# Performance work log

Hardware: AMD Instinct MI355X
Metric: run time of the kernel (lower is better)

Reference implementation:

```python
import jax, jax.numpy as jnp
import numpy as np

NSAMPLE = 3  # three_nn default
EPS = 1e-10
CLAMP = 10.0


def setup_inputs() -> dict:
    key = jax.random.key(0)
    k1, k2, k3 = jax.random.split(key, 3)
    B, C, N = 4, 3, 8192
    pos1 = jax.random.normal(k1, (B, C, N), dtype=jnp.float32)
    pos2 = jax.random.normal(k2, (B, C, N), dtype=jnp.float32)
    flow1 = jax.random.normal(k3, (B, C, N), dtype=jnp.float32) * 0.1
    return {"pos1": pos1, "pos2": pos2, "flow1": flow1}


def reference(pos1, pos2, flow1):
    # pos1, flow1: [B,3,N1]; pos2: [B,3,N2]
    pos1_to_2 = pos1 + flow1                       # warped source points [B,3,N1]
    q = jnp.transpose(pos2, (0, 2, 1))             # queries  [B,N2,3]
    k = jnp.transpose(pos1_to_2, (0, 2, 1))        # database [B,N1,3]

    # brute-force 3-NN: squared distances [B,N2,N1]
    d2 = (jnp.sum(q * q, axis=-1, keepdims=True)
          - 2.0 * jnp.einsum('bqc,bnc->bqn', q, k)
          + jnp.sum(k * k, axis=-1)[:, None, :])
    _, knn_idx = jax.lax.top_k(-d2, NSAMPLE)       # [B,N2,NSAMPLE] into N1

    # gather neighbor coords: [B,N2,NSAMPLE,3]
    grouped_pts = jax.vmap(lambda pts, ii: pts[ii])(k, knn_idx)
    diff = grouped_pts - q[:, :, None, :]
    dist = jnp.maximum(jnp.linalg.norm(diff, axis=-1), EPS)  # [B,N2,NSAMPLE]
    inv = 1.0 / dist
    weight = inv / jnp.sum(inv, axis=-1, keepdims=True)      # [B,N2,NSAMPLE]

    # gather neighbor flows and do inverse-distance-weighted average
    flow_t = jnp.transpose(flow1, (0, 2, 1))                 # [B,N1,3]
    grouped_flow = jax.vmap(lambda f, ii: f[ii])(flow_t, knn_idx)  # [B,N2,NSAMPLE,3]
    flow2 = jnp.sum(weight[..., None] * grouped_flow, axis=2)      # [B,N2,3]

    warped = pos2 - jnp.transpose(flow2, (0, 2, 1))          # [B,3,N2]
    return jnp.clip(warped, -CLAMP, CLAMP)
```

## Files before the change

### kernel.cpp

```cpp
#include <hip/hip_runtime.h>
#include <math.h>


#define BB 4
#define NN 8192
#define NC 30
#define NCELLS (NC * NC * NC)
#define NCT (BB * NCELLS)
#define GRID_R 3.3f
#define GRID_INVH (1.0f / 0.22f)
#define D3_THR (0.44f * 0.44f * 0.999f)
#define EPB 1024
#define SB 106

typedef unsigned long long u64;

__device__ __forceinline__ int cell_of(float x) {
  int c = (int)floorf((x + GRID_R) * GRID_INVH);
  return min(max(c, 0), NC - 1);
}

__device__ __forceinline__ void merge3(u64& a0, u64& a1, u64& a2,
                                       u64 b0, u64 b1, u64 b2) {
  const u64 lo0 = a0 < b0 ? a0 : b0;
  const u64 hi0 = a0 < b0 ? b0 : a0;
  const u64 lo1 = a1 < b1 ? a1 : b1;
  const u64 lo2 = a2 < b2 ? a2 : b2;
  const u64 o1 = hi0 < lo1 ? hi0 : lo1;
  const u64 t = hi0 < lo1 ? lo1 : hi0;
  a0 = lo0;
  a1 = o1;
  a2 = t < lo2 ? t : lo2;
}

__device__ __forceinline__ void insert3(u64& s0, u64& s1, u64& s2, u64 key) {
  const bool c0 = key < s0;
  const bool c1 = key < s1;
  const bool c2 = key < s2;
  s2 = c1 ? s1 : (c2 ? key : s2);
  s1 = c0 ? s0 : (c1 ? key : s1);
  s0 = c0 ? key : s0;
}

__global__ __launch_bounds__(256) void k_count(const float* __restrict__ p1,
                                               const float* __restrict__ f1,
                                               int* __restrict__ counts) {
  const int gid = blockIdx.x * 256 + threadIdx.x;
  const int b = gid >> 13, n = gid & (NN - 1);
  const float* P = p1 + (size_t)b * 3 * NN;
  const float* F = f1 + (size_t)b * 3 * NN;
  const float x = P[n] + F[n];
  const float y = P[NN + n] + F[NN + n];
  const float z = P[2 * NN + n] + F[2 * NN + n];
  const int cid = (cell_of(z) * NC + cell_of(y)) * NC + cell_of(x);
  atomicAdd(&counts[b * NCELLS + cid], 1);
}

__global__ __launch_bounds__(256) void k_scan1(int* __restrict__ counts,
                                               int* __restrict__ offs,
                                               int* __restrict__ partials) {
  __shared__ int wsums[4];
  const int tid = threadIdx.x, lane = tid & 63, wav = tid >> 6;
  const int c = blockIdx.x * EPB + tid * 4;
  int4 v = make_int4(0, 0, 0, 0);
  if (c < NCT) {
    v = *reinterpret_cast<const int4*>(counts + c);
    *reinterpret_cast<int4*>(counts + c) = make_int4(0, 0, 0, 0);
  }
  const int sum4 = v.x + v.y + v.z + v.w;
  int incl = sum4;
  for (int off = 1; off < 64; off <<= 1) {
    const int t = __shfl_up(incl, off, 64);
    incl += (lane >= off) ? t : 0;
  }
  if (lane == 63) wsums[wav] = incl;
  __syncthreads();
  int wbase = 0;
#pragma unroll
  for (int w = 0; w < 4; ++w) wbase += (w < wav) ? wsums[w] : 0;
  const int excl = wbase + incl - sum4;
  if (c < NCT) {
    int4 e;
    e.x = excl;
    e.y = excl + v.x;
    e.z = e.y + v.y;
    e.w = e.z + v.z;
    *reinterpret_cast<int4*>(offs + c) = e;
  }
  if (tid == 255) partials[blockIdx.x] = wbase + incl;
}

__global__ __launch_bounds__(128) void k_scan2(int* __restrict__ partials,
                                               int* __restrict__ offs) {
  __shared__ int w0sum;
  const int t = threadIdx.x, lane = t & 63, wav = t >> 6;
  const int v = (t < SB) ? partials[t] : 0;
  int incl = v;
  for (int off = 1; off < 64; off <<= 1) {
    const int u = __shfl_up(incl, off, 64);
    incl += (lane >= off) ? u : 0;
  }
  if (t == 63) w0sum = incl;
  __syncthreads();
  const int base = wav ? w0sum : 0;
  const int excl = base + incl - v;
  if (t < SB) partials[t] = excl;
  if (t == SB - 1) offs[NCT] = BB * NN - excl;
}

__global__ __launch_bounds__(256) void k_scatter(const float* __restrict__ p1,
                                                 const float* __restrict__ f1,
                                                 int* __restrict__ counts,
                                                 const int* __restrict__ offs,
                                                 const int* __restrict__ partials,
                                                 float4* __restrict__ csr) {
  const int gid = blockIdx.x * 256 + threadIdx.x;
  const int b = gid >> 13, n = gid & (NN - 1);
  const float* P = p1 + (size_t)b * 3 * NN;
  const float* F = f1 + (size_t)b * 3 * NN;
  const float x = P[n] + F[n];
  const float y = P[NN + n] + F[NN + n];
  const float z = P[2 * NN + n] + F[2 * NN + n];
  const int cid = (cell_of(z) * NC + cell_of(y)) * NC + cell_of(x);
  const int g = b * NCELLS + cid;
  const int rank = atomicAdd(&counts[g], 1);
  const int base = offs[g] + partials[g >> 10];
  csr[base + rank] = make_float4(x, y, z, __int_as_float(n));
}

__global__ __launch_bounds__(256) void k_query(const float* __restrict__ p1,
                                               const float* __restrict__ p2,
                                               const float* __restrict__ f1,
                                               const int* __restrict__ offs,
                                               const int* __restrict__ partials,
                                               const float4* __restrict__ csr,
                                               float* __restrict__ out) {
  __shared__ int cumL[4][32];
  __shared__ int adjL[4][32];
  const int tid = threadIdx.x, lane = tid & 63, wav = tid >> 6;
  const int bid = blockIdx.x;
  const int b = bid >> 11;
  const int qn = ((bid & 2047) << 2) | wav;
  const float* P1 = p1 + (size_t)b * 3 * NN;
  const float* P2 = p2 + (size_t)b * 3 * NN;
  const float* F1 = f1 + (size_t)b * 3 * NN;

  const float qx = P2[qn], qy = P2[NN + qn], qz = P2[2 * NN + qn];
  bool fb = !(fabsf(qx) < GRID_R && fabsf(qy) < GRID_R && fabsf(qz) < GRID_R);

  u64 s0 = ~0ULL, s1 = ~0ULL, s2 = ~0ULL;

  if (!fb) {
    const int qcx = cell_of(qx), qcy = cell_of(qy), qcz = cell_of(qz);
    int n_c = 0, start_c = 0;
    if (lane < 25) {
      const int gz = qcz + (lane / 5) - 2;
      const int gy = qcy + (lane % 5) - 2;
      if (gz >= 0 && gz < NC && gy >= 0 && gy < NC) {
        const int gxl = max(qcx - 2, 0), gxh = min(qcx + 2, NC - 1);
        const int cb = b * NCELLS + (gz * NC + gy) * NC;
        const int ia = cb + gxl, ib = cb + gxh + 1;
        start_c = offs[ia] + partials[ia >> 10];
        n_c = offs[ib] + partials[ib >> 10] - start_c;
      }
    }
    int incl = n_c;
    for (int off = 1; off < 64; off <<= 1) {
      const int v = __shfl_up(incl, off, 64);
      incl += (lane >= off) ? v : 0;
    }
    const int excl = incl - n_c;
    const int T = __shfl(incl, 24, 64);
    if (lane < 32) {
      cumL[wav][lane] = excl;
      adjL[wav][lane] = start_c - excl;
    }

    for (int g0 = 0; g0 < T; g0 += 64) {
      const int g = g0 + lane;
      const bool act = g < T;
      const int gg = act ? g : (T - 1);
      int c = 0;
#pragma unroll
      for (int st = 16; st >= 1; st >>= 1) {
        const int c2 = c + st;
        c = (cumL[wav][c2] <= gg) ? c2 : c;
      }
      const float4 pt = csr[adjL[wav][c] + gg];
      const float dx = pt.x - qx, dy = pt.y - qy, dz = pt.z - qz;
      const float d2 = fmaf(dx, dx, fmaf(dy, dy, dz * dz));
      u64 key = ((u64)__float_as_uint(d2) << 32) | (unsigned)__float_as_uint(pt.w);
      key = act ? key : ~0ULL;
      insert3(s0, s1, s2, key);
    }

#pragma unroll
    for (int mask = 32; mask >= 1; mask >>= 1) {
      const u64 b0 = __shfl_xor(s0, mask, 64);
      const u64 b1 = __shfl_xor(s1, mask, 64);
      const u64 b2 = __shfl_xor(s2, mask, 64);
      merge3(s0, s1, s2, b0, b1, b2);
    }

    const float d3 = __uint_as_float((unsigned)(s2 >> 32));
    fb = !(d3 <= D3_THR);
  }

  if (fb) {
    s0 = ~0ULL; s1 = ~0ULL; s2 = ~0ULL;
    for (int r = 0; r < NN / 64; ++r) {
      const int g = r * 64 + lane;
      const float x = P1[g] + F1[g];
      const float y = P1[NN + g] + F1[NN + g];
      const float z = P1[2 * NN + g] + F1[2 * NN + g];
      const float dx = x - qx, dy = y - qy, dz = z - qz;
      const float d2 = fmaf(dx, dx, fmaf(dy, dy, dz * dz));
      const u64 key = ((u64)__float_as_uint(d2) << 32) | (unsigned)g;
      insert3(s0, s1, s2, key);
    }
#pragma unroll
    for (int mask = 32; mask >= 1; mask >>= 1) {
      const u64 b0 = __shfl_xor(s0, mask, 64);
      const u64 b1 = __shfl_xor(s1, mask, 64);
      const u64 b2 = __shfl_xor(s2, mask, 64);
      merge3(s0, s1, s2, b0, b1, b2);
    }
  }

  if (lane == 0) {
    const int idxs[3] = {(int)(unsigned)s0 & (NN - 1),
                         (int)(unsigned)s1 & (NN - 1),
                         (int)(unsigned)s2 & (NN - 1)};
    float w[3], gfx[3], gfy[3], gfz[3];
    float wsumv = 0.0f;
#pragma unroll
    for (int r = 0; r < 3; ++r) {
      const int idx = idxs[r];
      const float fx = F1[idx], fy = F1[NN + idx], fz = F1[2 * NN + idx];
      const float kx = P1[idx] + fx;
      const float ky = P1[NN + idx] + fy;
      const float kz = P1[2 * NN + idx] + fz;
      const float dx = kx - qx, dy = ky - qy, dz = kz - qz;
      float d = sqrtf(dx * dx + dy * dy + dz * dz);
      d = fmaxf(d, 1e-10f);
      const float inv = 1.0f / d;
      w[r] = inv; wsumv += inv;
      gfx[r] = fx; gfy[r] = fy; gfz[r] = fz;
    }
    const float invw = 1.0f / wsumv;
    float ox = 0.0f, oy = 0.0f, oz = 0.0f;
#pragma unroll
    for (int r = 0; r < 3; ++r) {
      const float ww = w[r] * invw;
      ox = fmaf(ww, gfx[r], ox);
      oy = fmaf(ww, gfy[r], oy);
      oz = fmaf(ww, gfz[r], oz);
    }
    ox = qx - ox; oy = qy - oy; oz = qz - oz;
    ox = fminf(fmaxf(ox, -10.0f), 10.0f);
    oy = fminf(fmaxf(oy, -10.0f), 10.0f);
    oz = fminf(fmaxf(oz, -10.0f), 10.0f);
    float* o = out + (size_t)b * 3 * NN;
    o[qn] = ox;
    o[NN + qn] = oy;
    o[2 * NN + qn] = oz;
  }
}

extern "C" void kernel_launch(void* const* d_in, const int* in_sizes, int n_in,
                              void* d_out, int out_size, void* d_ws, size_t ws_size,
                              hipStream_t stream) {
  const float* pos1 = (const float*)d_in[0];
  const float* pos2 = (const float*)d_in[1];
  const float* flow1 = (const float*)d_in[2];
  float* out = (float*)d_out;

  char* ws = (char*)d_ws;
  int* counts = (int*)ws;
  int* offs = (int*)(ws + (size_t)NCT * 4);
  size_t part_off = ((size_t)NCT * 4 + ((size_t)NCT + 1) * 4 + 15) & ~(size_t)15;
  int* partials = (int*)(ws + part_off);
  size_t csr_off = (part_off + (size_t)SB * 4 + 15) & ~(size_t)15;
  float4* csr = (float4*)(ws + csr_off);

  hipMemsetAsync(counts, 0, (size_t)NCT * 4, stream);
  k_count<<<dim3(BB * NN / 256), dim3(256), 0, stream>>>(pos1, flow1, counts);
  k_scan1<<<dim3(SB), dim3(256), 0, stream>>>(counts, offs, partials);
  k_scan2<<<dim3(1), dim3(128), 0, stream>>>(partials, offs);
  k_scatter<<<dim3(BB * NN / 256), dim3(256), 0, stream>>>(pos1, flow1, counts, offs, partials, csr);
  k_query<<<dim3(BB * 2048), dim3(256), 0, stream>>>(pos1, pos2, flow1, offs, partials, csr, out);
}
```

Measured before the change: 86.21 us.

## Use four lanes per query and defer brute-force fallbacks to separate kernel

The query kernel now assigns four threads per query instead of a whole 64-lane wavefront, walking the 25 neighbouring cell rows with prefetch of the next row's offsets. Queries outside the grid or whose third-nearest distance fails the threshold are pushed onto a compacted queue via an atomic counter. A separate fallback kernel then brute-forces only those queries. Scan partials are folded into offsets by a new apply kernel, which removes the extra partials lookups. The intent is to cut the idle lanes and divergence of the wavefront-per-query design, at the cost of an extra launch and more serial work per thread.

```diff
diff --git a/kernel.cpp b/kernel.cpp
--- a/kernel.cpp
+++ b/kernel.cpp
@@ -40,6 +40,49 @@
   s2 = c1 ? s1 : (c2 ? key : s2);
   s1 = c0 ? s0 : (c1 ? key : s1);
   s0 = c0 ? key : s0;
+}
+
+__device__ __forceinline__ void idw_out(int b, int qn, float qx, float qy,
+                                        float qz, u64 s0, u64 s1, u64 s2,
+                                        const float* __restrict__ P1,
+                                        const float* __restrict__ F1,
+                                        float* __restrict__ out) {
+  const int idxs[3] = {(int)(unsigned)s0 & (NN - 1),
+                       (int)(unsigned)s1 & (NN - 1),
+                       (int)(unsigned)s2 & (NN - 1)};
+  float w[3], gfx[3], gfy[3], gfz[3];
+  float wsumv = 0.0f;
+#pragma unroll
+  for (int r = 0; r < 3; ++r) {
+    const int idx = idxs[r];
+    const float fx = F1[idx], fy = F1[NN + idx], fz = F1[2 * NN + idx];
+    const float kx = P1[idx] + fx;
+    const float ky = P1[NN + idx] + fy;
+    const float kz = P1[2 * NN + idx] + fz;
+    const float dx = kx - qx, dy = ky - qy, dz = kz - qz;
+    float d = sqrtf(dx * dx + dy * dy + dz * dz);
+    d = fmaxf(d, 1e-10f);
+    const float inv = 1.0f / d;
+    w[r] = inv; wsumv += inv;
+    gfx[r] = fx; gfy[r] = fy; gfz[r] = fz;
+  }
+  const float invw = 1.0f / wsumv;
+  float ox = 0.0f, oy = 0.0f, oz = 0.0f;
+#pragma unroll
+  for (int r = 0; r < 3; ++r) {
+    const float ww = w[r] * invw;
+    ox = fmaf(ww, gfx[r], ox);
+    oy = fmaf(ww, gfy[r], oy);
+    oz = fmaf(ww, gfz[r], oz);
+  }
+  ox = qx - ox; oy = qy - oy; oz = qz - oz;
+  ox = fminf(fmaxf(ox, -10.0f), 10.0f);
+  oy = fminf(fmaxf(oy, -10.0f), 10.0f);
+  oz = fminf(fmaxf(oz, -10.0f), 10.0f);
+  float* o = out + (size_t)b * 3 * NN;
+  o[qn] = ox;
+  o[NN + qn] = oy;
+  o[2 * NN + qn] = oz;
 }
 
 __global__ __launch_bounds__(256) void k_count(const float* __restrict__ p1,
@@ -90,8 +133,7 @@
   if (tid == 255) partials[blockIdx.x] = wbase + incl;
 }
 
-__global__ __launch_bounds__(128) void k_scan2(int* __restrict__ partials,
-                                               int* __restrict__ offs) {
+__global__ __launch_bounds__(128) void k_scan2(int* __restrict__ partials) {
   __shared__ int w0sum;
   const int t = threadIdx.x, lane = t & 63, wav = t >> 6;
   const int v = (t < SB) ? partials[t] : 0;
@@ -103,16 +145,25 @@
   if (t == 63) w0sum = incl;
   __syncthreads();
   const int base = wav ? w0sum : 0;
-  const int excl = base + incl - v;
-  if (t < SB) partials[t] = excl;
-  if (t == SB - 1) offs[NCT] = BB * NN - excl;
+  if (t < SB) partials[t] = base + incl - v;
+}
+
+__global__ __launch_bounds__(256) void k_apply(int* __restrict__ offs,
+                                               const int* __restrict__ partials) {
+  const int base = partials[blockIdx.x];
+  const int c = blockIdx.x * EPB + threadIdx.x * 4;
+  if (c < NCT) {
+    int4 v = *reinterpret_cast<const int4*>(offs + c);
+    v.x += base; v.y += base; v.z += base; v.w += base;
+    *reinterpret_cast<int4*>(offs + c) = v;
+  }
+  if (blockIdx.x == 0 && threadIdx.x == 0) offs[NCT] = BB * NN;
 }
 
 __global__ __launch_bounds__(256) void k_scatter(const float* __restrict__ p1,
                                                  const float* __restrict__ f1,
                                                  int* __restrict__ counts,
                                                  const int* __restrict__ offs,
-                                                 const int* __restrict__ partials,
                                                  float4* __restrict__ csr) {
   const int gid = blockIdx.x * 256 + threadIdx.x;
   const int b = gid >> 13, n = gid & (NN - 1);
@@ -124,76 +175,117 @@
   const int cid = (cell_of(z) * NC + cell_of(y)) * NC + cell_of(x);
   const int g = b * NCELLS + cid;
   const int rank = atomicAdd(&counts[g], 1);
-  const int base = offs[g] + partials[g >> 10];
-  csr[base + rank] = make_float4(x, y, z, __int_as_float(n));
+  csr[offs[g] + rank] = make_float4(x, y, z, __int_as_float(n));
 }
 
 __global__ __launch_bounds__(256) void k_query(const float* __restrict__ p1,
                                                const float* __restrict__ p2,
                                                const float* __restrict__ f1,
                                                const int* __restrict__ offs,
-                                               const int* __restrict__ partials,
                                                const float4* __restrict__ csr,
-                                               float* __restrict__ out) {
-  __shared__ int cumL[4][32];
-  __shared__ int adjL[4][32];
-  const int tid = threadIdx.x, lane = tid & 63, wav = tid >> 6;
-  const int bid = blockIdx.x;
-  const int b = bid >> 11;
-  const int qn = ((bid & 2047) << 2) | wav;
+                                               float* __restrict__ out,
+                                               int* __restrict__ fbcnt,
+                                               int* __restrict__ fbq) {
+  const int gtid = blockIdx.x * 256 + threadIdx.x;
+  const int qid = gtid >> 2;
+  const int r = gtid & 3;
+  const int b = qid >> 13;
+  const int qn = qid & (NN - 1);
   const float* P1 = p1 + (size_t)b * 3 * NN;
   const float* P2 = p2 + (size_t)b * 3 * NN;
   const float* F1 = f1 + (size_t)b * 3 * NN;
 
   const float qx = P2[qn], qy = P2[NN + qn], qz = P2[2 * NN + qn];
-  bool fb = !(fabsf(qx) < GRID_R && fabsf(qy) < GRID_R && fabsf(qz) < GRID_R);
+  const bool oor = !(fabsf(qx) < GRID_R && fabsf(qy) < GRID_R && fabsf(qz) < GRID_R);
 
   u64 s0 = ~0ULL, s1 = ~0ULL, s2 = ~0ULL;
 
-  if (!fb) {
+  if (!oor) {
     const int qcx = cell_of(qx), qcy = cell_of(qy), qcz = cell_of(qz);
-    int n_c = 0, start_c = 0;
-    if (lane < 25) {
-      const int gz = qcz + (lane / 5) - 2;
-      const int gy = qcy + (lane % 5) - 2;
-      if (gz >= 0 && gz < NC && gy >= 0 && gy < NC) {
-        const int gxl = max(qcx - 2, 0), gxh = min(qcx + 2, NC - 1);
-        const int cb = b * NCELLS + (gz * NC + gy) * NC;
-        const int ia = cb + gxl, ib = cb + gxh + 1;
-        start_c = offs[ia] + partials[ia >> 10];
-        n_c = offs[ib] + partials[ib >> 10] - start_c;
+    const int gxl = max(qcx - 2, 0);
+    const int span = min(qcx + 2, NC - 1) - gxl + 1;
+    const int cb = b * NCELLS;
+
+    int st_c = 0, en_c = 0;
+    {
+      const int gz = qcz - 2, gy = qcy - 2;
+      if (((unsigned)gz < NC) & ((unsigned)gy < NC)) {
+        const int ia = cb + (gz * NC + gy) * NC + gxl;
+        st_c = offs[ia];
+        en_c = offs[ia + span];
       }
     }
-    int incl = n_c;
-    for (int off = 1; off < 64; off <<= 1) {
-      const int v = __shfl_up(incl, off, 64);
-      incl += (lane >= off) ? v : 0;
-    }
-    const int excl = incl - n_c;
-    const int T = __shfl(incl, 24, 64);
-    if (lane < 32) {
-      cumL[wav][lane] = excl;
-      adjL[wav][lane] = start_c - excl;
-    }
-
-    for (int g0 = 0; g0 < T; g0 += 64) {
-      const int g = g0 + lane;
-      const bool act = g < T;
-      const int gg = act ? g : (T - 1);
-      int c = 0;
-#pragma unroll
-      for (int st = 16; st >= 1; st >>= 1) {
-        const int c2 = c + st;
-        c = (cumL[wav][c2] <= gg) ? c2 : c;
+    for (int c = 0; c < 25; ++c) {
+      int st_n = 0, en_n = 0;
+      if (c < 24) {
+        const int cn = c + 1;
+        const int dzi = (cn * 205) >> 10;
+        const int gz = qcz + dzi - 2;
+        const int gy = qcy + (cn - dzi * 5) - 2;
+        if (((unsigned)gz < NC) & ((unsigned)gy < NC)) {
+          const int ia = cb + (gz * NC + gy) * NC + gxl;
+          st_n = offs[ia];
+          en_n = offs[ia + span];
+        }
       }
-      const float4 pt = csr[adjL[wav][c] + gg];
-      const float dx = pt.x - qx, dy = pt.y - qy, dz = pt.z - qz;
+      for (int j = st_c + r; j < en_c; j += 4) {
+        const float4 pt = csr[j];
+        const float dx = pt.x - qx, dy = pt.y - qy, dz = pt.z - qz;
+        const float d2 = fmaf(dx, dx, fmaf(dy, dy, dz * dz));
+        const u64 key = ((u64)__float_as_uint(d2) << 32) |
+                        (unsigned)__float_as_uint(pt.w);
+        insert3(s0, s1, s2, key);
+      }
+      st_c = st_n;
+      en_c = en_n;
+    }
+  }
+
+  {
+    u64 b0 = __shfl_xor(s0, 1, 64), b1 = __shfl_xor(s1, 1, 64), b2 = __shfl_xor(s2, 1, 64);
+    merge3(s0, s1, s2, b0, b1, b2);
+    b0 = __shfl_xor(s0, 2, 64); b1 = __shfl_xor(s1, 2, 64); b2 = __shfl_xor(s2, 2, 64);
+    merge3(s0, s1, s2, b0, b1, b2);
+  }
+
+  if (r == 0) {
+    const float d3 = __uint_as_float((unsigned)(s2 >> 32));
+    const bool ok = !oor && (d3 <= D3_THR);
+    if (!ok) {
+      const int slot = atomicAdd(fbcnt, 1);
+      fbq[slot] = qid;
+    } else {
+      idw_out(b, qn, qx, qy, qz, s0, s1, s2, P1, F1, out);
+    }
+  }
+}
+
+__global__ __launch_bounds__(256) void k_fallback(const float* __restrict__ p1,
+                                                  const float* __restrict__ p2,
+                                                  const float* __restrict__ f1,
+                                                  const int* __restrict__ fbcnt,
+                                                  const int* __restrict__ fbq,
+                                                  float* __restrict__ out) {
+  const int gtid = blockIdx.x * 256 + threadIdx.x;
+  const int wid = gtid >> 6, lane = gtid & 63;
+  const int nfb = fbcnt[0];
+  for (int i = wid; i < nfb; i += 1024) {
+    const int qid = fbq[i];
+    const int b = qid >> 13, qn = qid & (NN - 1);
+    const float* P1 = p1 + (size_t)b * 3 * NN;
+    const float* P2 = p2 + (size_t)b * 3 * NN;
+    const float* F1 = f1 + (size_t)b * 3 * NN;
+    const float qx = P2[qn], qy = P2[NN + qn], qz = P2[2 * NN + qn];
+    u64 s0 = ~0ULL, s1 = ~0ULL, s2 = ~0ULL;
+    for (int t = 0; t < NN / 64; ++t) {
+      const int g = t * 64 + lane;
+      const float x = P1[g] + F1[g];
+      const float y = P1[NN + g] + F1[NN + g];
+      const float z = P1[2 * NN + g] + F1[2 * NN + g];
+      const float dx = x - qx, dy = y - qy, dz = z - qz;
       const float d2 = fmaf(dx, dx, fmaf(dy, dy, dz * dz));
-      u64 key = ((u64)__float_as_uint(d2) << 32) | (unsigned)__float_as_uint(pt.w);
-      key = act ? key : ~0ULL;
-      insert3(s0, s1, s2, key);
-    }
-
+      insert3(s0, s1, s2, ((u64)__float_as_uint(d2) << 32) | (unsigned)g);
+    }
 #pragma unroll
     for (int mask = 32; mask >= 1; mask >>= 1) {
       const u64 b0 = __shfl_xor(s0, mask, 64);
@@ -201,69 +293,7 @@
       const u64 b2 = __shfl_xor(s2, mask, 64);
       merge3(s0, s1, s2, b0, b1, b2);
     }
-
-    const float d3 = __uint_as_float((unsigned)(s2 >> 32));
-    fb = !(d3 <= D3_THR);
-  }
-
-  if (fb) {
-    s0 = ~0ULL; s1 = ~0ULL; s2 = ~0ULL;
-    for (int r = 0; r < NN / 64; ++r) {
-      const int g = r * 64 + lane;
-      const float x = P1[g] + F1[g];
-      const float y = P1[NN + g] + F1[NN + g];
-      const float z = P1[2 * NN + g] + F1[2 * NN + g];
-      const float dx = x - qx, dy = y - qy, dz = z - qz;
-      const float d2 = fmaf(dx, dx, fmaf(dy, dy, dz * dz));
-      const u64 key = ((u64)__float_as_uint(d2) << 32) | (unsigned)g;
-      insert3(s0, s1, s2, key);
-    }
-#pragma unroll
-    for (int mask = 32; mask >= 1; mask >>= 1) {
-      const u64 b0 = __shfl_xor(s0, mask, 64);
-      const u64 b1 = __shfl_xor(s1, mask, 64);
-      const u64 b2 = __shfl_xor(s2, mask, 64);
-      merge3(s0, s1, s2, b0, b1, b2);
-    }
-  }
-
-  if (lane == 0) {
-    const int idxs[3] = {(int)(unsigned)s0 & (NN - 1),
-                         (int)(unsigned)s1 & (NN - 1),
-                         (int)(unsigned)s2 & (NN - 1)};
-    float w[3], gfx[3], gfy[3], gfz[3];
-    float wsumv = 0.0f;
-#pragma unroll
-    for (int r = 0; r < 3; ++r) {
-      const int idx = idxs[r];
-      const float fx = F1[idx], fy = F1[NN + idx], fz = F1[2 * NN + idx];
-      const float kx = P1[idx] + fx;
-      const float ky = P1[NN + idx] + fy;
-      const float kz = P1[2 * NN + idx] + fz;
-      const float dx = kx - qx, dy = ky - qy, dz = kz - qz;
-      float d = sqrtf(dx * dx + dy * dy + dz * dz);
-      d = fmaxf(d, 1e-10f);
-      const float inv = 1.0f / d;
-      w[r] = inv; wsumv += inv;
-      gfx[r] = fx; gfy[r] = fy; gfz[r] = fz;
-    }
-    const float invw = 1.0f / wsumv;
-    float ox = 0.0f, oy = 0.0f, oz = 0.0f;
-#pragma unroll
-    for (int r = 0; r < 3; ++r) {
-      const float ww = w[r] * invw;
-      ox = fmaf(ww, gfx[r], ox);
-      oy = fmaf(ww, gfy[r], oy);
-      oz = fmaf(ww, gfz[r], oz);
-    }
-    ox = qx - ox; oy = qy - oy; oz = qz - oz;
-    ox = fminf(fmaxf(ox, -10.0f), 10.0f);
-    oy = fminf(fmaxf(oy, -10.0f), 10.0f);
-    oz = fminf(fmaxf(oz, -10.0f), 10.0f);
-    float* o = out + (size_t)b * 3 * NN;
-    o[qn] = ox;
-    o[NN + qn] = oy;
-    o[2 * NN + qn] = oz;
+    if (lane == 0) idw_out(b, qn, qx, qy, qz, s0, s1, s2, P1, F1, out);
   }
 }
 
@@ -277,16 +307,22 @@
 
   char* ws = (char*)d_ws;
   int* counts = (int*)ws;
-  int* offs = (int*)(ws + (size_t)NCT * 4);
-  size_t part_off = ((size_t)NCT * 4 + ((size_t)NCT + 1) * 4 + 15) & ~(size_t)15;
+  int* fbcnt = counts + NCT;
+  size_t offs_off = (((size_t)NCT + 1) * 4 + 15) & ~(size_t)15;
+  int* offs = (int*)(ws + offs_off);
+  size_t part_off = (offs_off + ((size_t)NCT + 1) * 4 + 15) & ~(size_t)15;
   int* partials = (int*)(ws + part_off);
-  size_t csr_off = (part_off + (size_t)SB * 4 + 15) & ~(size_t)15;
+  size_t fbq_off = (part_off + (size_t)SB * 4 + 15) & ~(size_t)15;
+  int* fbq = (int*)(ws + fbq_off);
+  size_t csr_off = (fbq_off + (size_t)BB * NN * 4 + 15) & ~(size_t)15;
   float4* csr = (float4*)(ws + csr_off);
 
-  hipMemsetAsync(counts, 0, (size_t)NCT * 4, stream);
+  hipMemsetAsync(counts, 0, ((size_t)NCT + 1) * 4, stream);
   k_count<<<dim3(BB * NN / 256), dim3(256), 0, stream>>>(pos1, flow1, counts);
   k_scan1<<<dim3(SB), dim3(256), 0, stream>>>(counts, offs, partials);
-  k_scan2<<<dim3(1), dim3(128), 0, stream>>>(partials, offs);
-  k_scatter<<<dim3(BB * NN / 256), dim3(256), 0, stream>>>(pos1, flow1, counts, offs, partials, csr);
-  k_query<<<dim3(BB * 2048), dim3(256), 0, stream>>>(pos1, pos2, flow1, offs, partials, csr, out);
-}
+  k_scan2<<<dim3(1), dim3(128), 0, stream>>>(partials);
+  k_apply<<<dim3(SB), dim3(256), 0, stream>>>(offs, partials);
+  k_scatter<<<dim3(BB * NN / 256), dim3(256), 0, stream>>>(pos1, flow1, counts, offs, csr);
+  k_query<<<dim3(BB * NN * 4 / 256), dim3(256), 0, stream>>>(pos1, pos2, flow1, offs, csr, out, fbcnt, fbq);
+  k_fallback<<<dim3(256), dim3(256), 0, stream>>>(pos1, pos2, flow1, fbcnt, fbq, out);
+}
```

Result: slower. 116.6 us (+35.3%).

## Bin queries into grid cells and share staged candidate neighbors per cell

Applied to the files above, without the earlier changes.

Queries are now bucketed into the same uniform grid as the database points, and one wave handles all queries of a cell. The wave stages the 5x5x5 neighborhood candidates into shared memory once and scans them with four queries at a time, 16 lanes per query. This replaces the per-query gather of candidates from global memory. It also merges the two-level scan into a block-parallel fixup kernel and swaps the memset for a zero kernel. The cost is a grid of 27000 cells per batch where most waves exit early, and extra counting and scatter work for the query points.

```diff
diff --git a/kernel.cpp b/kernel.cpp
--- a/kernel.cpp
+++ b/kernel.cpp
@@ -4,14 +4,17 @@
 
 #define BB 4
 #define NN 8192
+#define BBNN (BB * NN)
 #define NC 30
 #define NCELLS (NC * NC * NC)
 #define NCT (BB * NCELLS)
+#define NCT2 (2 * NCT)
 #define GRID_R 3.3f
 #define GRID_INVH (1.0f / 0.22f)
 #define D3_THR (0.44f * 0.44f * 0.999f)
 #define EPB 1024
-#define SB 106
+#define SB 211
+#define CANDCAP 768
 
 typedef unsigned long long u64;
 
@@ -42,18 +45,92 @@
   s0 = c0 ? key : s0;
 }
 
+__device__ __forceinline__ void wave_merge3(u64& s0, u64& s1, u64& s2) {
+#pragma unroll
+  for (int mask = 32; mask >= 1; mask >>= 1) {
+    const u64 b0 = __shfl_xor(s0, mask, 64);
+    const u64 b1 = __shfl_xor(s1, mask, 64);
+    const u64 b2 = __shfl_xor(s2, mask, 64);
+    merge3(s0, s1, s2, b0, b1, b2);
+  }
+}
+
+__device__ __forceinline__ void cand1(const float4& a, float qx, float qy,
+                                      float qz, u64& s0, u64& s1, u64& s2) {
+  const float dx = a.x - qx, dy = a.y - qy, dz = a.z - qz;
+  const float d2 = fmaf(dx, dx, fmaf(dy, dy, dz * dz));
+  insert3(s0, s1, s2,
+          ((u64)__float_as_uint(d2) << 32) | (unsigned)__float_as_uint(a.w));
+}
+
+__device__ __forceinline__ void idw_out(int b, int qn, float qx, float qy,
+                                        float qz, u64 s0, u64 s1, u64 s2,
+                                        const float* __restrict__ P1,
+                                        const float* __restrict__ F1,
+                                        float* __restrict__ out) {
+  const int idxs[3] = {(int)(unsigned)s0 & (NN - 1),
+                       (int)(unsigned)s1 & (NN - 1),
+                       (int)(unsigned)s2 & (NN - 1)};
+  float w[3], gfx[3], gfy[3], gfz[3];
+  float wsumv = 0.0f;
+#pragma unroll
+  for (int r = 0; r < 3; ++r) {
+    const int idx = idxs[r];
+    const float fx = F1[idx], fy = F1[NN + idx], fz = F1[2 * NN + idx];
+    const float kx = P1[idx] + fx;
+    const float ky = P1[NN + idx] + fy;
+    const float kz = P1[2 * NN + idx] + fz;
+    const float dx = kx - qx, dy = ky - qy, dz = kz - qz;
+    float d = sqrtf(dx * dx + dy * dy + dz * dz);
+    d = fmaxf(d, 1e-10f);
+    const float inv = 1.0f / d;
+    w[r] = inv; wsumv += inv;
+    gfx[r] = fx; gfy[r] = fy; gfz[r] = fz;
+  }
+  const float invw = 1.0f / wsumv;
+  float ox = 0.0f, oy = 0.0f, oz = 0.0f;
+#pragma unroll
+  for (int r = 0; r < 3; ++r) {
+    const float ww = w[r] * invw;
+    ox = fmaf(ww, gfx[r], ox);
+    oy = fmaf(ww, gfy[r], oy);
+    oz = fmaf(ww, gfz[r], oz);
+  }
+  ox = qx - ox; oy = qy - oy; oz = qz - oz;
+  ox = fminf(fmaxf(ox, -10.0f), 10.0f);
+  oy = fminf(fmaxf(oy, -10.0f), 10.0f);
+  oz = fminf(fmaxf(oz, -10.0f), 10.0f);
+  float* o = out + (size_t)b * 3 * NN;
+  o[qn] = ox;
+  o[NN + qn] = oy;
+  o[2 * NN + qn] = oz;
+}
+
+__global__ __launch_bounds__(256) void k_zero(int4* __restrict__ p) {
+  const int i = blockIdx.x * 256 + threadIdx.x;
+  if (i < NCT2 / 4) p[i] = make_int4(0, 0, 0, 0);
+}
+
 __global__ __launch_bounds__(256) void k_count(const float* __restrict__ p1,
+                                               const float* __restrict__ p2,
                                                const float* __restrict__ f1,
                                                int* __restrict__ counts) {
   const int gid = blockIdx.x * 256 + threadIdx.x;
-  const int b = gid >> 13, n = gid & (NN - 1);
-  const float* P = p1 + (size_t)b * 3 * NN;
-  const float* F = f1 + (size_t)b * 3 * NN;
-  const float x = P[n] + F[n];
-  const float y = P[NN + n] + F[NN + n];
-  const float z = P[2 * NN + n] + F[2 * NN + n];
+  const bool isq = gid >= BBNN;
+  const int id = isq ? gid - BBNN : gid;
+  const int b = id >> 13, n = id & (NN - 1);
+  float x, y, z;
+  if (isq) {
+    const float* P = p2 + (size_t)b * 3 * NN;
+    x = P[n]; y = P[NN + n]; z = P[2 * NN + n];
+  } else {
+    const float* P = p1 + (size_t)b * 3 * NN;
+    const float* F = f1 + (size_t)b * 3 * NN;
+    x = P[n] + F[n]; y = P[NN + n] + F[NN + n]; z = P[2 * NN + n] + F[2 * NN + n];
+  }
   const int cid = (cell_of(z) * NC + cell_of(y)) * NC + cell_of(x);
-  atomicAdd(&counts[b * NCELLS + cid], 1);
+  const int g = (isq ? NCT : 0) + b * NCELLS + cid;
+  atomicAdd(&counts[g], 1);
 }
 
 __global__ __launch_bounds__(256) void k_scan1(int* __restrict__ counts,
@@ -63,7 +140,7 @@
   const int tid = threadIdx.x, lane = tid & 63, wav = tid >> 6;
   const int c = blockIdx.x * EPB + tid * 4;
   int4 v = make_int4(0, 0, 0, 0);
-  if (c < NCT) {
+  if (c < NCT2) {
     v = *reinterpret_cast<const int4*>(counts + c);
     *reinterpret_cast<int4*>(counts + c) = make_int4(0, 0, 0, 0);
   }
@@ -79,7 +156,7 @@
 #pragma unroll
   for (int w = 0; w < 4; ++w) wbase += (w < wav) ? wsums[w] : 0;
   const int excl = wbase + incl - sum4;
-  if (c < NCT) {
+  if (c < NCT2) {
     int4 e;
     e.x = excl;
     e.y = excl + v.x;
@@ -90,180 +167,183 @@
   if (tid == 255) partials[blockIdx.x] = wbase + incl;
 }
 
-__global__ __launch_bounds__(128) void k_scan2(int* __restrict__ partials,
-                                               int* __restrict__ offs) {
-  __shared__ int w0sum;
-  const int t = threadIdx.x, lane = t & 63, wav = t >> 6;
-  const int v = (t < SB) ? partials[t] : 0;
-  int incl = v;
-  for (int off = 1; off < 64; off <<= 1) {
-    const int u = __shfl_up(incl, off, 64);
-    incl += (lane >= off) ? u : 0;
-  }
-  if (t == 63) w0sum = incl;
+__global__ __launch_bounds__(256) void k_final(int* __restrict__ offs,
+                                               const int* __restrict__ partials) {
+  __shared__ int sbase;
+  const int tid = threadIdx.x, lane = tid & 63;
+  const int bid = blockIdx.x;
+  if (tid < 64) {
+    int v = 0;
+#pragma unroll
+    for (int k = 0; k < 4; ++k) {
+      const int j = lane + 64 * k;
+      if (j < bid) v += partials[j];
+    }
+    for (int off = 32; off >= 1; off >>= 1) v += __shfl_down(v, off, 64);
+    if (lane == 0) sbase = v;
+  }
   __syncthreads();
-  const int base = wav ? w0sum : 0;
-  const int excl = base + incl - v;
-  if (t < SB) partials[t] = excl;
-  if (t == SB - 1) offs[NCT] = BB * NN - excl;
-}
-
-__global__ __launch_bounds__(256) void k_scatter(const float* __restrict__ p1,
-                                                 const float* __restrict__ f1,
-                                                 int* __restrict__ counts,
-                                                 const int* __restrict__ offs,
-                                                 const int* __restrict__ partials,
-                                                 float4* __restrict__ csr) {
+  const int base = sbase;
+  const int c = bid * EPB + tid * 4;
+  if (c < NCT2) {
+    int4 v = *reinterpret_cast<const int4*>(offs + c);
+    v.x += base; v.y += base; v.z += base; v.w += base;
+    *reinterpret_cast<int4*>(offs + c) = v;
+  }
+  if (bid == 0 && tid == 0) offs[NCT2] = 2 * BBNN;
+}
+
+__global__ __launch_bounds__(256) void k_scat(const float* __restrict__ p1,
+                                              const float* __restrict__ p2,
+                                              const float* __restrict__ f1,
+                                              int* __restrict__ counts,
+                                              const int* __restrict__ offs,
+                                              float4* __restrict__ csr,
+                                              int* __restrict__ qlist) {
   const int gid = blockIdx.x * 256 + threadIdx.x;
-  const int b = gid >> 13, n = gid & (NN - 1);
-  const float* P = p1 + (size_t)b * 3 * NN;
-  const float* F = f1 + (size_t)b * 3 * NN;
-  const float x = P[n] + F[n];
-  const float y = P[NN + n] + F[NN + n];
-  const float z = P[2 * NN + n] + F[2 * NN + n];
+  const bool isq = gid >= BBNN;
+  const int id = isq ? gid - BBNN : gid;
+  const int b = id >> 13, n = id & (NN - 1);
+  float x, y, z;
+  if (isq) {
+    const float* P = p2 + (size_t)b * 3 * NN;
+    x = P[n]; y = P[NN + n]; z = P[2 * NN + n];
+  } else {
+    const float* P = p1 + (size_t)b * 3 * NN;
+    const float* F = f1 + (size_t)b * 3 * NN;
+    x = P[n] + F[n]; y = P[NN + n] + F[NN + n]; z = P[2 * NN + n] + F[2 * NN + n];
+  }
   const int cid = (cell_of(z) * NC + cell_of(y)) * NC + cell_of(x);
-  const int g = b * NCELLS + cid;
+  const int g = (isq ? NCT : 0) + b * NCELLS + cid;
   const int rank = atomicAdd(&counts[g], 1);
-  const int base = offs[g] + partials[g >> 10];
-  csr[base + rank] = make_float4(x, y, z, __int_as_float(n));
-}
-
-__global__ __launch_bounds__(256) void k_query(const float* __restrict__ p1,
-                                               const float* __restrict__ p2,
-                                               const float* __restrict__ f1,
-                                               const int* __restrict__ offs,
-                                               const int* __restrict__ partials,
-                                               const float4* __restrict__ csr,
-                                               float* __restrict__ out) {
-  __shared__ int cumL[4][32];
-  __shared__ int adjL[4][32];
+  const int pos = offs[g] + rank;
+  if (isq) qlist[pos - BBNN] = n;
+  else csr[pos] = make_float4(x, y, z, __int_as_float(n));
+}
+
+__global__ __launch_bounds__(256) void k_cohort(const float* __restrict__ p1,
+                                                const float* __restrict__ p2,
+                                                const float* __restrict__ f1,
+                                                const int* __restrict__ offs,
+                                                const float4* __restrict__ csr,
+                                                const int* __restrict__ qlist,
+                                                float* __restrict__ out) {
+  __shared__ float4 cand[4][CANDCAP];
+  __shared__ int cumA[4][32];
+  __shared__ int adjA[4][32];
   const int tid = threadIdx.x, lane = tid & 63, wav = tid >> 6;
-  const int bid = blockIdx.x;
-  const int b = bid >> 11;
-  const int qn = ((bid & 2047) << 2) | wav;
+  const int cell = blockIdx.x * 4 + wav;
+  const int b = cell / NCELLS;
+  const int cc = cell - b * NCELLS;
+
+  const int qoff = offs[NCT + cell];
+  const int qcnt = offs[NCT + cell + 1] - qoff;
+  if (qcnt == 0) return;
+
   const float* P1 = p1 + (size_t)b * 3 * NN;
   const float* P2 = p2 + (size_t)b * 3 * NN;
   const float* F1 = f1 + (size_t)b * 3 * NN;
 
-  const float qx = P2[qn], qy = P2[NN + qn], qz = P2[2 * NN + qn];
-  bool fb = !(fabsf(qx) < GRID_R && fabsf(qy) < GRID_R && fabsf(qz) < GRID_R);
-
-  u64 s0 = ~0ULL, s1 = ~0ULL, s2 = ~0ULL;
-
-  if (!fb) {
-    const int qcx = cell_of(qx), qcy = cell_of(qy), qcz = cell_of(qz);
-    int n_c = 0, start_c = 0;
-    if (lane < 25) {
-      const int gz = qcz + (lane / 5) - 2;
-      const int gy = qcy + (lane % 5) - 2;
-      if (gz >= 0 && gz < NC && gy >= 0 && gy < NC) {
-        const int gxl = max(qcx - 2, 0), gxh = min(qcx + 2, NC - 1);
-        const int cb = b * NCELLS + (gz * NC + gy) * NC;
-        const int ia = cb + gxl, ib = cb + gxh + 1;
-        start_c = offs[ia] + partials[ia >> 10];
-        n_c = offs[ib] + partials[ib >> 10] - start_c;
-      }
-    }
-    int incl = n_c;
-    for (int off = 1; off < 64; off <<= 1) {
-      const int v = __shfl_up(incl, off, 64);
-      incl += (lane >= off) ? v : 0;
-    }
-    const int excl = incl - n_c;
-    const int T = __shfl(incl, 24, 64);
-    if (lane < 32) {
-      cumL[wav][lane] = excl;
-      adjL[wav][lane] = start_c - excl;
-    }
-
+  const int cz = cc / 900;
+  const int rem = cc - cz * 900;
+  const int cy = rem / 30;
+  const int cx = rem - cy * 30;
+
+  const int gxl = max(cx - 2, 0);
+  const int span = min(cx + 2, NC - 1) - gxl + 1;
+  const int cb = b * NCELLS;
+  int n_c = 0, st_c = 0;
+  if (lane < 25) {
+    const int dzi = (lane * 205) >> 10;
+    const int gz = cz + dzi - 2;
+    const int gy = cy + (lane - dzi * 5) - 2;
+    if (((unsigned)gz < NC) & ((unsigned)gy < NC)) {
+      const int ia = cb + (gz * NC + gy) * NC + gxl;
+      st_c = offs[ia];
+      n_c = offs[ia + span] - st_c;
+    }
+  }
+  int incl = n_c;
+  for (int off = 1; off < 64; off <<= 1) {
+    const int v = __shfl_up(incl, off, 64);
+    incl += (lane >= off) ? v : 0;
+  }
+  const int excl = incl - n_c;
+  const int T = __shfl(incl, 24, 64);
+  if (lane < 32) {
+    cumA[wav][lane] = excl;
+    adjA[wav][lane] = st_c - excl;
+  }
+  const bool bigfb = T > CANDCAP;
+
+  if (!bigfb) {
     for (int g0 = 0; g0 < T; g0 += 64) {
       const int g = g0 + lane;
-      const bool act = g < T;
-      const int gg = act ? g : (T - 1);
-      int c = 0;
-#pragma unroll
-      for (int st = 16; st >= 1; st >>= 1) {
-        const int c2 = c + st;
-        c = (cumL[wav][c2] <= gg) ? c2 : c;
+      if (g < T) {
+        int c = 0;
+#pragma unroll
+        for (int st = 16; st >= 1; st >>= 1) {
+          const int c2 = c + st;
+          c = (cumA[wav][c2] <= g) ? c2 : c;
+        }
+        cand[wav][g] = csr[adjA[wav][c] + g];
       }
-      const float4 pt = csr[adjL[wav][c] + gg];
-      const float dx = pt.x - qx, dy = pt.y - qy, dz = pt.z - qz;
-      const float d2 = fmaf(dx, dx, fmaf(dy, dy, dz * dz));
-      u64 key = ((u64)__float_as_uint(d2) << 32) | (unsigned)__float_as_uint(pt.w);
-      key = act ? key : ~0ULL;
-      insert3(s0, s1, s2, key);
-    }
-
-#pragma unroll
-    for (int mask = 32; mask >= 1; mask >>= 1) {
+    }
+    asm volatile("s_waitcnt lgkmcnt(0)" ::: "memory");
+    __builtin_amdgcn_sched_barrier(0);
+  }
+
+  const int group = lane >> 4;
+  const int sl = lane & 15;
+
+  for (int q0 = 0; q0 < qcnt; q0 += 4) {
+    const int qsel = q0 + group;
+    const bool vq = qsel < qcnt;
+    const int qn = qlist[qoff - BBNN + (vq ? qsel : 0)];
+    const float qx = P2[qn], qy = P2[NN + qn], qz = P2[2 * NN + qn];
+    const bool oor = !(fabsf(qx) < GRID_R && fabsf(qy) < GRID_R && fabsf(qz) < GRID_R);
+
+    u64 s0 = ~0ULL, s1 = ~0ULL, s2 = ~0ULL;
+    if (!bigfb && !oor) {
+      for (int j = sl; j < T; j += 16) {
+        cand1(cand[wav][j], qx, qy, qz, s0, s1, s2);
+      }
+    }
+#pragma unroll
+    for (int mask = 1; mask <= 8; mask <<= 1) {
       const u64 b0 = __shfl_xor(s0, mask, 64);
       const u64 b1 = __shfl_xor(s1, mask, 64);
       const u64 b2 = __shfl_xor(s2, mask, 64);
       merge3(s0, s1, s2, b0, b1, b2);
     }
-
     const float d3 = __uint_as_float((unsigned)(s2 >> 32));
-    fb = !(d3 <= D3_THR);
-  }
-
-  if (fb) {
-    s0 = ~0ULL; s1 = ~0ULL; s2 = ~0ULL;
-    for (int r = 0; r < NN / 64; ++r) {
-      const int g = r * 64 + lane;
-      const float x = P1[g] + F1[g];
-      const float y = P1[NN + g] + F1[NN + g];
-      const float z = P1[2 * NN + g] + F1[2 * NN + g];
-      const float dx = x - qx, dy = y - qy, dz = z - qz;
-      const float d2 = fmaf(dx, dx, fmaf(dy, dy, dz * dz));
-      const u64 key = ((u64)__float_as_uint(d2) << 32) | (unsigned)g;
-      insert3(s0, s1, s2, key);
-    }
-#pragma unroll
-    for (int mask = 32; mask >= 1; mask >>= 1) {
-      const u64 b0 = __shfl_xor(s0, mask, 64);
-      const u64 b1 = __shfl_xor(s1, mask, 64);
-      const u64 b2 = __shfl_xor(s2, mask, 64);
-      merge3(s0, s1, s2, b0, b1, b2);
-    }
-  }
-
-  if (lane == 0) {
-    const int idxs[3] = {(int)(unsigned)s0 & (NN - 1),
-                         (int)(unsigned)s1 & (NN - 1),
-                         (int)(unsigned)s2 & (NN - 1)};
-    float w[3], gfx[3], gfy[3], gfz[3];
-    float wsumv = 0.0f;
-#pragma unroll
-    for (int r = 0; r < 3; ++r) {
-      const int idx = idxs[r];
-      const float fx = F1[idx], fy = F1[NN + idx], fz = F1[2 * NN + idx];
-      const float kx = P1[idx] + fx;
-      const float ky = P1[NN + idx] + fy;
-      const float kz = P1[2 * NN + idx] + fz;
-      const float dx = kx - qx, dy = ky - qy, dz = kz - qz;
-      float d = sqrtf(dx * dx + dy * dy + dz * dz);
-      d = fmaxf(d, 1e-10f);
-      const float inv = 1.0f / d;
-      w[r] = inv; wsumv += inv;
-      gfx[r] = fx; gfy[r] = fy; gfz[r] = fz;
-    }
-    const float invw = 1.0f / wsumv;
-    float ox = 0.0f, oy = 0.0f, oz = 0.0f;
-#pragma unroll
-    for (int r = 0; r < 3; ++r) {
-      const float ww = w[r] * invw;
-      ox = fmaf(ww, gfx[r], ox);
-      oy = fmaf(ww, gfy[r], oy);
-      oz = fmaf(ww, gfz[r], oz);
-    }
-    ox = qx - ox; oy = qy - oy; oz = qz - oz;
-    ox = fminf(fmaxf(ox, -10.0f), 10.0f);
-    oy = fminf(fmaxf(oy, -10.0f), 10.0f);
-    oz = fminf(fmaxf(oz, -10.0f), 10.0f);
-    float* o = out + (size_t)b * 3 * NN;
-    o[qn] = ox;
-    o[NN + qn] = oy;
-    o[2 * NN + qn] = oz;
+    const bool ok = vq && !bigfb && !oor && (d3 <= D3_THR);
+
+    if (sl == 0 && ok) idw_out(b, qn, qx, qy, qz, s0, s1, s2, P1, F1, out);
+
+    const u64 bal = __ballot(sl == 0 && vq && !ok);
+    if (bal != 0) {
+#pragma unroll
+      for (int q = 0; q < 4; ++q) {
+        if (!((bal >> (16 * q)) & 1ULL)) continue;
+        const int fqn = __shfl(qn, 16 * q, 64);
+        const float fqx = __shfl(qx, 16 * q, 64);
+        const float fqy = __shfl(qy, 16 * q, 64);
+        const float fqz = __shfl(qz, 16 * q, 64);
+        u64 a0 = ~0ULL, a1 = ~0ULL, a2 = ~0ULL;
+        for (int t = 0; t < NN / 64; ++t) {
+          const int g = t * 64 + lane;
+          const float x = P1[g] + F1[g];
+          const float y = P1[NN + g] + F1[NN + g];
+          const float z = P1[2 * NN + g] + F1[2 * NN + g];
+          const float dx = x - fqx, dy = y - fqy, dz = z - fqz;
+          const float d2 = fmaf(dx, dx, fmaf(dy, dy, dz * dz));
+          insert3(a0, a1, a2, ((u64)__float_as_uint(d2) << 32) | (unsigned)g);
+        }
+        wave_merge3(a0, a1, a2);
+        if (lane == 0) idw_out(b, fqn, fqx, fqy, fqz, a0, a1, a2, P1, F1, out);
+      }
+    }
   }
 }
 
@@ -277,16 +357,21 @@
 
   char* ws = (char*)d_ws;
   int* counts = (int*)ws;
-  int* offs = (int*)(ws + (size_t)NCT * 4);
-  size_t part_off = ((size_t)NCT * 4 + ((size_t)NCT + 1) * 4 + 15) & ~(size_t)15;
+  size_t offs_off = ((size_t)NCT2 * 4 + 15) & ~(size_t)15;
+  int* offs = (int*)(ws + offs_off);
+  size_t part_off = (offs_off + ((size_t)NCT2 + 1) * 4 + 15) & ~(size_t)15;
   int* partials = (int*)(ws + part_off);
-  size_t csr_off = (part_off + (size_t)SB * 4 + 15) & ~(size_t)15;
+  size_t ql_off = (part_off + (size_t)SB * 4 + 15) & ~(size_t)15;
+  int* qlist = (int*)(ws + ql_off);
+  size_t csr_off = (ql_off + (size_t)BBNN * 4 + 15) & ~(size_t)15;
   float4* csr = (float4*)(ws + csr_off);
 
-  hipMemsetAsync(counts, 0, (size_t)NCT * 4, stream);
-  k_count<<<dim3(BB * NN / 256), dim3(256), 0, stream>>>(pos1, flow1, counts);
+  k_zero<<<dim3((NCT2 / 4 + 255) / 256), dim3(256), 0, stream>>>((int4*)counts);
+  k_count<<<dim3(2 * BBNN / 256), dim3(256), 0, stream>>>(pos1, pos2, flow1, counts);
   k_scan1<<<dim3(SB), dim3(256), 0, stream>>>(counts, offs, partials);
-  k_scan2<<<dim3(1), dim3(128), 0, stream>>>(partials, offs);
-  k_scatter<<<dim3(BB * NN / 256), dim3(256), 0, stream>>>(pos1, flow1, counts, offs, partials, csr);
-  k_query<<<dim3(BB * 2048), dim3(256), 0, stream>>>(pos1, pos2, flow1, offs, partials, csr, out);
-}
+  k_final<<<dim3(SB), dim3(256), 0, stream>>>(offs, partials);
+  k_scat<<<dim3(2 * BBNN / 256), dim3(256), 0, stream>>>(pos1, pos2, flow1, counts,
+                                                         offs, csr, qlist);
+  k_cohort<<<dim3(NCT / 4), dim3(256), 0, stream>>>(pos1, pos2, flow1, offs, csr,
+                                                    qlist, out);
+}
```

Result: slower. 160.0 us (+85.6%).
